# Optimization experiments

Measured on AMD Instinct MI355X. Metric: run time of the kernel, lower is better.

## Reference

```python
import jax, jax.numpy as jnp
import numpy as np

B, S, D, H = 2, 4096, 512, 4  # batch, seq, hidden, broadcast heads (mask shape)
SCALE = np.float32(np.sqrt(D))  # original divides by np.sqrt(self.d)


def setup_inputs() -> dict:
    key = jax.random.key(0)
    ks = jax.random.split(key, 7)
    lim = np.float32(1.0 / np.sqrt(D))  # torch Linear default init range
    return {
        "q": jax.random.normal(ks[0], (B, S, D), dtype=jnp.float32),
        "k": jax.random.normal(ks[1], (B, S, D), dtype=jnp.float32),
        "v": jax.random.normal(ks[2], (B, S, D), dtype=jnp.float32),
        "Wq": jax.random.uniform(ks[3], (D, D), jnp.float32, -lim, lim),
        "bq": jax.random.uniform(ks[4], (D,), jnp.float32, -lim, lim),
        "Wv": jax.random.uniform(ks[5], (D, D), jnp.float32, -lim, lim),
        "bv": jax.random.uniform(ks[6], (D,), jnp.float32, -lim, lim),
    }


def reference(q, k, v, Wq, bq, Wv, bv):
    # Q projection (original only projects q; key/value raw k is used for scores)
    Q = q @ Wq.T + bq                                   # [B,S,D]
    scores = jnp.einsum("bsd,btd->bst", Q, k) / SCALE   # [B,S,S]
    # zero attn_mask of shape [B,H,S,S] broadcasts scores to [B,H,S,S]
    scores = jnp.broadcast_to(scores[:, None, :, :], (B, H, S, S))
    attn = jax.nn.softmax(scores, axis=-1)              # [B,H,S,S]
    V = v @ Wv.T + bv                                   # [B,S,D]
    out = jnp.einsum("bhst,btd->bhsd", attn, V)         # [B,H,S,D]
    return out
```

## Files before the change

### kernel.cpp

```cpp
#include <hip/hip_runtime.h>
#include <math.h>

#define SEQ 4096
#define DIM 512
#define NBATCH 2

typedef __bf16 bf16;
typedef __bf16 bf16x8 __attribute__((ext_vector_type(8)));
typedef __bf16 bf16x4 __attribute__((ext_vector_type(4)));
typedef float  f32x4  __attribute__((ext_vector_type(4)));

#define GLOAD_LDS16(g, l)                                                              \
  __builtin_amdgcn_global_load_lds((__attribute__((address_space(1))) void*)(g),       \
                                   (__attribute__((address_space(3))) void*)(l), 16, 0, 0)

static const long NQ_ = (long)NBATCH * SEQ * DIM;
static const long NW_ = (long)DIM * DIM;
#define QSCALE 0.04419417382415922f

__device__ __forceinline__ void cvt4(const float* __restrict__ s, bf16* __restrict__ d) {
  f32x4 x = *(const f32x4*)s;
  bf16x4 y;
  y[0] = (bf16)x[0]; y[1] = (bf16)x[1]; y[2] = (bf16)x[2]; y[3] = (bf16)x[3];
  *(bf16x4*)d = y;
}

__global__ __launch_bounds__(256)
void cast5(const float* __restrict__ q, const float* __restrict__ k,
           const float* __restrict__ v, const float* __restrict__ Wq,
           const float* __restrict__ Wv,
           bf16* __restrict__ qb, bf16* __restrict__ kb, bf16* __restrict__ vb,
           bf16* __restrict__ wqb, bf16* __restrict__ wvb) {
  long tid = blockIdx.x * 256L + threadIdx.x;
  long nth = gridDim.x * 256L;
  for (long i = tid * 4; i < NQ_; i += nth * 4) {
    cvt4(q + i, qb + i);
    cvt4(k + i, kb + i);
    cvt4(v + i, vb + i);
  }
  for (long i = tid * 4; i < NW_; i += nth * 4) {
    cvt4(Wq + i, wqb + i);
    cvt4(Wv + i, wvb + i);
  }
}

__global__ __launch_bounds__(256)
void zero_f32(float* __restrict__ p, int n) {
  int i = blockIdx.x * 256 + threadIdx.x;
  if (i < n) p[i] = 0.0f;
}

template <int OUT>
__global__ __launch_bounds__(512, 2)
void gemm8(const bf16* __restrict__ A, const bf16* __restrict__ Bt,
           void* __restrict__ Cv, const float* __restrict__ bias0,
           const float* __restrict__ bias1, float* __restrict__ rowsum,
           int N, int K, long sB) {
  __shared__ __align__(16) bf16 lA[2][256 * 64];
  __shared__ __align__(16) bf16 lB[2][128 * 64];
  const int t = threadIdx.x;
  const int l = t & 63, w = t >> 6;

  const unsigned bid = blockIdx.y * gridDim.x + blockIdx.x;
  const unsigned nwg = gridDim.x * gridDim.y;
  const unsigned q8 = nwg >> 3;
  const unsigned swz = (bid & 7) * q8 + (bid >> 3);
  const long m0 = (long)(swz % gridDim.x) * 256;
  const long n0 = (long)(swz / gridDim.x) * 128;

  const int z = blockIdx.z;
  if constexpr (OUT == 0) {
    A += (long)z * NQ_;
    Bt += (long)z * NW_;
  } else {
    Bt += (m0 >> 12) * sB;
  }

  const int wr = (w >> 1) * 64;
  const int wc = (w & 1) * 64;
  const int lr = l & 15, lg = l >> 4;

  const bf16* gA[4];
  const bf16* gB[2];
#pragma unroll
  for (int i = 0; i < 4; ++i) {
    int s = i * 512 + t, row = s >> 3, kc = (s & 7) ^ (row & 7);
    gA[i] = A + (m0 + row) * (long)K + kc * 8;
  }
#pragma unroll
  for (int i = 0; i < 2; ++i) {
    int s = i * 512 + t, row = s >> 3, kc = (s & 7) ^ (row & 7);
    gB[i] = Bt + (n0 + row) * (long)K + kc * 8;
  }

  int offA[4][2], offB[4][2];
#pragma unroll
  for (int m = 0; m < 4; ++m)
#pragma unroll
    for (int ks = 0; ks < 2; ++ks)
      offA[m][ks] = (wr + m * 16 + lr) * 64 + (((ks * 4 + lg) ^ (lr & 7)) * 8);
#pragma unroll
  for (int n = 0; n < 4; ++n)
#pragma unroll
    for (int ks = 0; ks < 2; ++ks)
      offB[n][ks] = (wc + n * 16 + lr) * 64 + (((ks * 4 + lg) ^ (lr & 7)) * 8);

  auto stage6 = [&](long koff, bf16* dA, bf16* dB) {
#pragma unroll
    for (int i = 0; i < 4; ++i) GLOAD_LDS16(gA[i] + koff, dA + (i * 512 + w * 64) * 8);
#pragma unroll
    for (int i = 0; i < 2; ++i) GLOAD_LDS16(gB[i] + koff, dB + (i * 512 + w * 64) * 8);
  };

  f32x4 acc[4][4] = {};
  const int NT = K >> 6;

  stage6(0, lA[0], lB[0]);
  stage6(64, lA[1], lB[1]);
  asm volatile("s_waitcnt vmcnt(6)" ::: "memory");
  __builtin_amdgcn_sched_barrier(0);
  __builtin_amdgcn_s_barrier();
  __builtin_amdgcn_sched_barrier(0);

  for (int tt = 0; tt < NT; ++tt) {
    const int cur = tt & 1;
    const bf16* bufA = lA[cur];
    const bf16* bufB = lB[cur];
    bf16x8 a0[4], b0[4];
#pragma unroll
    for (int m = 0; m < 4; ++m) a0[m] = *(const bf16x8*)(bufA + offA[m][0]);
#pragma unroll
    for (int n = 0; n < 4; ++n) b0[n] = *(const bf16x8*)(bufB + offB[n][0]);
    asm volatile("s_waitcnt lgkmcnt(0)" ::: "memory");
    __builtin_amdgcn_sched_barrier(0);
    __builtin_amdgcn_s_setprio(1);
#pragma unroll
    for (int m = 0; m < 4; ++m)
#pragma unroll
      for (int n = 0; n < 4; ++n)
        acc[m][n] = __builtin_amdgcn_mfma_f32_16x16x32_bf16(a0[m], b0[n], acc[m][n], 0, 0, 0);
    __builtin_amdgcn_s_setprio(0);
    bf16x8 a1[4], b1[4];
#pragma unroll
    for (int m = 0; m < 4; ++m) a1[m] = *(const bf16x8*)(bufA + offA[m][1]);
#pragma unroll
    for (int n = 0; n < 4; ++n) b1[n] = *(const bf16x8*)(bufB + offB[n][1]);
    asm volatile("s_waitcnt lgkmcnt(0)" ::: "memory");
    __builtin_amdgcn_sched_barrier(0);
    __builtin_amdgcn_s_barrier();
    __builtin_amdgcn_sched_barrier(0);
    if (tt + 2 < NT) stage6((long)(tt + 2) * 64, lA[cur], lB[cur]);
    __builtin_amdgcn_s_setprio(1);
#pragma unroll
    for (int m = 0; m < 4; ++m)
#pragma unroll
      for (int n = 0; n < 4; ++n)
        acc[m][n] = __builtin_amdgcn_mfma_f32_16x16x32_bf16(a1[m], b1[n], acc[m][n], 0, 0, 0);
    __builtin_amdgcn_s_setprio(0);
    if (tt + 2 < NT) {
      asm volatile("s_waitcnt vmcnt(6)" ::: "memory");
    } else if (tt + 1 < NT) {
      asm volatile("s_waitcnt vmcnt(0)" ::: "memory");
    }
    if (tt + 1 < NT) {
      __builtin_amdgcn_sched_barrier(0);
      __builtin_amdgcn_s_barrier();
      __builtin_amdgcn_sched_barrier(0);
    }
  }

  if constexpr (OUT == 0) {
    if (z == 0) {
      bf16* C = (bf16*)Cv;
#pragma unroll
      for (int n = 0; n < 4; ++n) {
        const long col = n0 + wc + n * 16 + lr;
        const float bcol = bias0[col];
#pragma unroll
        for (int m = 0; m < 4; ++m) {
          const long rowb = m0 + wr + m * 16 + lg * 4;
#pragma unroll
          for (int r = 0; r < 4; ++r)
            C[(rowb + r) * (long)DIM + col] = (bf16)((acc[m][n][r] + bcol) * QSCALE);
        }
      }
    } else {
      bf16* Vt = (bf16*)Cv + NQ_;
#pragma unroll
      for (int n = 0; n < 4; ++n) {
        const long col = n0 + wc + n * 16 + lr;
        const float bcol = bias1[col];
#pragma unroll
        for (int m = 0; m < 4; ++m) {
          const long rowb = m0 + wr + m * 16 + lg * 4;
#pragma unroll
          for (int r = 0; r < 4; ++r) {
            long gr = rowb + r, bb = gr >> 12, ss = gr & 4095;
            Vt[bb * (long)(DIM * SEQ) + col * (long)SEQ + ss] = (bf16)(acc[m][n][r] + bcol);
          }
        }
      }
    }
  } else if constexpr (OUT == 1) {
    bf16* C = (bf16*)Cv;
#pragma unroll
    for (int m = 0; m < 4; ++m) {
      const long rowb = m0 + wr + m * 16 + lg * 4;
#pragma unroll
      for (int r = 0; r < 4; ++r) {
        float rsum = 0.0f;
#pragma unroll
        for (int n = 0; n < 4; ++n) {
          const long col = n0 + wc + n * 16 + lr;
          float e = __expf(acc[m][n][r]);
          bf16 eb = (bf16)e;
          C[(rowb + r) * (long)N + col] = eb;
          rsum += (float)eb;
        }
        rsum += __shfl_xor(rsum, 1);
        rsum += __shfl_xor(rsum, 2);
        rsum += __shfl_xor(rsum, 4);
        rsum += __shfl_xor(rsum, 8);
        if (lr == 0) atomicAdd(rowsum + rowb + r, rsum);
      }
    }
  } else {
    float* o = (float*)Cv;
#pragma unroll
    for (int m = 0; m < 4; ++m) {
      const long rowb = m0 + wr + m * 16 + lg * 4;
#pragma unroll
      for (int r = 0; r < 4; ++r) {
        const long gr = rowb + r, bb = gr >> 12, ss = gr & 4095;
        const float inv = 1.0f / rowsum[gr];
        float* p0 = o + bb * (4L * SEQ * DIM) + ss * (long)DIM;
#pragma unroll
        for (int n = 0; n < 4; ++n) {
          const long col = n0 + wc + n * 16 + lr;
          float vv = acc[m][n][r] * inv;
          p0[col] = vv;
          p0[col + 1L * SEQ * DIM] = vv;
          p0[col + 2L * SEQ * DIM] = vv;
          p0[col + 3L * SEQ * DIM] = vv;
        }
      }
    }
  }
}

extern "C" void kernel_launch(void* const* d_in, const int* in_sizes, int n_in,
                              void* d_out, int out_size, void* d_ws, size_t ws_size,
                              hipStream_t stream) {
  const float* q  = (const float*)d_in[0];
  const float* k  = (const float*)d_in[1];
  const float* v  = (const float*)d_in[2];
  const float* Wq = (const float*)d_in[3];
  const float* bq = (const float*)d_in[4];
  const float* Wv = (const float*)d_in[5];
  const float* bv = (const float*)d_in[6];
  float* outp = (float*)d_out;

  bf16* Qbf = (bf16*)d_ws;
  bf16* Vt  = Qbf + NQ_;
  bf16* Kbf = Vt + NQ_;
  bf16* Wqb = Kbf + NQ_;
  bf16* Wvb = Wqb + NW_;
  bf16* Sbuf = Wvb + NW_;
  const size_t baseBytes = (size_t)((char*)Sbuf - (char*)d_ws);
  const bool batched = ws_size >= baseBytes + 2ULL * SEQ * SEQ * 2;
  bf16* qb = Sbuf;
  bf16* vb = Sbuf + NQ_;
  float* rowsum = (float*)Wqb;

  const long sQK = (long)SEQ * DIM;
  const long sO  = 4L * SEQ * DIM;

  cast5<<<dim3(2048), dim3(256), 0, stream>>>(q, k, v, Wq, Wv, qb, Kbf, vb, Wqb, Wvb);
  gemm8<0><<<dim3(32, 4, 2), dim3(512), 0, stream>>>(
      qb, Wqb, Qbf, bq, bv, nullptr, 512, 512, 0);
  if (batched) {
    zero_f32<<<dim3(32), dim3(256), 0, stream>>>(rowsum, NBATCH * SEQ);
    gemm8<1><<<dim3(32, 32, 1), dim3(512), 0, stream>>>(
        Qbf, Kbf, Sbuf, nullptr, nullptr, rowsum, 4096, 512, sQK);
    gemm8<2><<<dim3(32, 4, 1), dim3(512), 0, stream>>>(
        Sbuf, Vt, outp, nullptr, nullptr, rowsum, 512, 4096, sQK);
  } else {
    for (int b = 0; b < 2; ++b) {
      zero_f32<<<dim3(16), dim3(256), 0, stream>>>(rowsum, SEQ);
      gemm8<1><<<dim3(16, 32, 1), dim3(512), 0, stream>>>(
          Qbf + b * sQK, Kbf + b * sQK, Sbuf, nullptr, nullptr, rowsum, 4096, 512, sQK);
      gemm8<2><<<dim3(16, 4, 1), dim3(512), 0, stream>>>(
          Sbuf, Vt + b * sQK, outp + b * sO, nullptr, nullptr, rowsum, 512, 4096, sQK);
    }
  }
}
```

Before: 278.1 us.

## Template GEMM on tile shape with triple-buffered BK=32 LDS pipeline

Replaces the fixed 256x128 double-buffered BK=64 GEMM with a templated BMxBN kernel that uses a three-stage LDS ring of BK=32 tiles. Each iteration issues the next global-to-LDS load before the MFMAs and needs only one barrier per step. Tile shapes are chosen per stage: 128x128 for the projections and the PV product, which doubles the grid, and 256x256 for the score GEMM. The catch is more loop iterations with smaller K slices, and the bigger score tiles hold more accumulators, which may limit occupancy.

```diff
diff --git a/kernel.cpp b/kernel.cpp
--- a/kernel.cpp
+++ b/kernel.cpp
@@ -13,6 +13,8 @@
 #define GLOAD_LDS16(g, l)                                                              \
   __builtin_amdgcn_global_load_lds((__attribute__((address_space(1))) void*)(g),       \
                                    (__attribute__((address_space(3))) void*)(l), 16, 0, 0)
+
+#define VMCNT(n) asm volatile("s_waitcnt vmcnt(" #n ")" ::: "memory")
 
 static const long NQ_ = (long)NBATCH * SEQ * DIM;
 static const long NW_ = (long)DIM * DIM;
@@ -50,23 +52,31 @@
   if (i < n) p[i] = 0.0f;
 }
 
-template <int OUT>
-__global__ __launch_bounds__(512, 2)
-void gemm8(const bf16* __restrict__ A, const bf16* __restrict__ Bt,
+template <int BM, int BN, int OUT>
+__global__ __launch_bounds__(512, (BM == 256 ? 2 : 4))
+void gemm3(const bf16* __restrict__ A, const bf16* __restrict__ Bt,
            void* __restrict__ Cv, const float* __restrict__ bias0,
            const float* __restrict__ bias1, float* __restrict__ rowsum,
            int N, int K, long sB) {
-  __shared__ __align__(16) bf16 lA[2][256 * 64];
-  __shared__ __align__(16) bf16 lB[2][128 * 64];
+  constexpr int MF = BM / 32;
+  constexpr int NF = BN / 64;
+  constexpr int LA = BM / 128;
+  constexpr int LB = BN / 128;
+  constexpr int NLD = LA + LB;
+  constexpr int ASZ = BM * 32;
+  constexpr int BSZ = BN * 32;
+  __shared__ __align__(16) bf16 lds[3][ASZ + BSZ];
+
   const int t = threadIdx.x;
   const int l = t & 63, w = t >> 6;
+  const int lr = l & 15, lg = l >> 4;
 
   const unsigned bid = blockIdx.y * gridDim.x + blockIdx.x;
   const unsigned nwg = gridDim.x * gridDim.y;
   const unsigned q8 = nwg >> 3;
   const unsigned swz = (bid & 7) * q8 + (bid >> 3);
-  const long m0 = (long)(swz % gridDim.x) * 256;
-  const long n0 = (long)(swz / gridDim.x) * 128;
+  const long m0 = (long)(swz % gridDim.x) * BM;
+  const long n0 = (long)(swz / gridDim.x) * BN;
 
   const int z = blockIdx.z;
   if constexpr (OUT == 0) {
@@ -76,127 +86,132 @@
     Bt += (m0 >> 12) * sB;
   }
 
-  const int wr = (w >> 1) * 64;
-  const int wc = (w & 1) * 64;
-  const int lr = l & 15, lg = l >> 4;
-
-  const bf16* gA[4];
-  const bf16* gB[2];
-#pragma unroll
-  for (int i = 0; i < 4; ++i) {
-    int s = i * 512 + t, row = s >> 3, kc = (s & 7) ^ (row & 7);
-    gA[i] = A + (m0 + row) * (long)K + kc * 8;
-  }
-#pragma unroll
-  for (int i = 0; i < 2; ++i) {
-    int s = i * 512 + t, row = s >> 3, kc = (s & 7) ^ (row & 7);
-    gB[i] = Bt + (n0 + row) * (long)K + kc * 8;
-  }
-
-  int offA[4][2], offB[4][2];
-#pragma unroll
-  for (int m = 0; m < 4; ++m)
-#pragma unroll
-    for (int ks = 0; ks < 2; ++ks)
-      offA[m][ks] = (wr + m * 16 + lr) * 64 + (((ks * 4 + lg) ^ (lr & 7)) * 8);
-#pragma unroll
-  for (int n = 0; n < 4; ++n)
-#pragma unroll
-    for (int ks = 0; ks < 2; ++ks)
-      offB[n][ks] = (wc + n * 16 + lr) * 64 + (((ks * 4 + lg) ^ (lr & 7)) * 8);
-
-  auto stage6 = [&](long koff, bf16* dA, bf16* dB) {
-#pragma unroll
-    for (int i = 0; i < 4; ++i) GLOAD_LDS16(gA[i] + koff, dA + (i * 512 + w * 64) * 8);
-#pragma unroll
-    for (int i = 0; i < 2; ++i) GLOAD_LDS16(gB[i] + koff, dB + (i * 512 + w * 64) * 8);
+  const int wr = (w >> 2) * (BM / 2);
+  const int wc = (w & 3) * (BN / 4);
+
+  const bf16* gA[LA];
+  const bf16* gB[LB];
+#pragma unroll
+  for (int i = 0; i < LA; ++i) {
+    int s = i * 512 + t, row = s >> 2, c = (s & 3) ^ ((row >> 1) & 3);
+    gA[i] = A + (m0 + row) * (long)K + c * 8;
+  }
+#pragma unroll
+  for (int i = 0; i < LB; ++i) {
+    int s = i * 512 + t, row = s >> 2, c = (s & 3) ^ ((row >> 1) & 3);
+    gB[i] = Bt + (n0 + row) * (long)K + c * 8;
+  }
+
+  int offA[MF], offB[NF];
+#pragma unroll
+  for (int mf = 0; mf < MF; ++mf)
+    offA[mf] = (wr + mf * 16 + lr) * 32 + ((lg ^ ((lr >> 1) & 3)) * 8);
+#pragma unroll
+  for (int nf = 0; nf < NF; ++nf)
+    offB[nf] = ASZ + (wc + nf * 16 + lr) * 32 + ((lg ^ ((lr >> 1) & 3)) * 8);
+
+  auto stage = [&](int tt, int bidx) {
+    const long ko = (long)tt * 32;
+#pragma unroll
+    for (int i = 0; i < LA; ++i)
+      GLOAD_LDS16(gA[i] + ko, &lds[bidx][(i * 512 + w * 64) * 8]);
+#pragma unroll
+    for (int i = 0; i < LB; ++i)
+      GLOAD_LDS16(gB[i] + ko, &lds[bidx][ASZ + (i * 512 + w * 64) * 8]);
   };
 
-  f32x4 acc[4][4] = {};
-  const int NT = K >> 6;
-
-  stage6(0, lA[0], lB[0]);
-  stage6(64, lA[1], lB[1]);
-  asm volatile("s_waitcnt vmcnt(6)" ::: "memory");
+  f32x4 acc[MF][NF] = {};
+  const int NT = K >> 5;
+
+  stage(0, 0);
+  stage(1, 1);
+  if constexpr (NLD == 4) VMCNT(4); else VMCNT(2);
   __builtin_amdgcn_sched_barrier(0);
   __builtin_amdgcn_s_barrier();
   __builtin_amdgcn_sched_barrier(0);
 
-  for (int tt = 0; tt < NT; ++tt) {
-    const int cur = tt & 1;
-    const bf16* bufA = lA[cur];
-    const bf16* bufB = lB[cur];
-    bf16x8 a0[4], b0[4];
-#pragma unroll
-    for (int m = 0; m < 4; ++m) a0[m] = *(const bf16x8*)(bufA + offA[m][0]);
-#pragma unroll
-    for (int n = 0; n < 4; ++n) b0[n] = *(const bf16x8*)(bufB + offB[n][0]);
-    asm volatile("s_waitcnt lgkmcnt(0)" ::: "memory");
-    __builtin_amdgcn_sched_barrier(0);
+  int cur = 0, stg = 2;
+  for (int tt = 0; tt < NT - 2; ++tt) {
+    bf16x8 af[MF], bfn[NF];
+#pragma unroll
+    for (int mf = 0; mf < MF; ++mf) af[mf] = *(const bf16x8*)(&lds[cur][offA[mf]]);
+#pragma unroll
+    for (int nf = 0; nf < NF; ++nf) bfn[nf] = *(const bf16x8*)(&lds[cur][offB[nf]]);
+    stage(tt + 2, stg);
     __builtin_amdgcn_s_setprio(1);
 #pragma unroll
-    for (int m = 0; m < 4; ++m)
-#pragma unroll
-      for (int n = 0; n < 4; ++n)
-        acc[m][n] = __builtin_amdgcn_mfma_f32_16x16x32_bf16(a0[m], b0[n], acc[m][n], 0, 0, 0);
+    for (int mf = 0; mf < MF; ++mf)
+#pragma unroll
+      for (int nf = 0; nf < NF; ++nf)
+        acc[mf][nf] = __builtin_amdgcn_mfma_f32_16x16x32_bf16(af[mf], bfn[nf], acc[mf][nf], 0, 0, 0);
     __builtin_amdgcn_s_setprio(0);
-    bf16x8 a1[4], b1[4];
-#pragma unroll
-    for (int m = 0; m < 4; ++m) a1[m] = *(const bf16x8*)(bufA + offA[m][1]);
-#pragma unroll
-    for (int n = 0; n < 4; ++n) b1[n] = *(const bf16x8*)(bufB + offB[n][1]);
-    asm volatile("s_waitcnt lgkmcnt(0)" ::: "memory");
+    if constexpr (NLD == 4) VMCNT(4); else VMCNT(2);
     __builtin_amdgcn_sched_barrier(0);
     __builtin_amdgcn_s_barrier();
     __builtin_amdgcn_sched_barrier(0);
-    if (tt + 2 < NT) stage6((long)(tt + 2) * 64, lA[cur], lB[cur]);
+    cur = (cur == 2) ? 0 : cur + 1;
+    stg = (stg == 2) ? 0 : stg + 1;
+  }
+  {
+    bf16x8 af[MF], bfn[NF];
+#pragma unroll
+    for (int mf = 0; mf < MF; ++mf) af[mf] = *(const bf16x8*)(&lds[cur][offA[mf]]);
+#pragma unroll
+    for (int nf = 0; nf < NF; ++nf) bfn[nf] = *(const bf16x8*)(&lds[cur][offB[nf]]);
     __builtin_amdgcn_s_setprio(1);
 #pragma unroll
-    for (int m = 0; m < 4; ++m)
-#pragma unroll
-      for (int n = 0; n < 4; ++n)
-        acc[m][n] = __builtin_amdgcn_mfma_f32_16x16x32_bf16(a1[m], b1[n], acc[m][n], 0, 0, 0);
+    for (int mf = 0; mf < MF; ++mf)
+#pragma unroll
+      for (int nf = 0; nf < NF; ++nf)
+        acc[mf][nf] = __builtin_amdgcn_mfma_f32_16x16x32_bf16(af[mf], bfn[nf], acc[mf][nf], 0, 0, 0);
     __builtin_amdgcn_s_setprio(0);
-    if (tt + 2 < NT) {
-      asm volatile("s_waitcnt vmcnt(6)" ::: "memory");
-    } else if (tt + 1 < NT) {
-      asm volatile("s_waitcnt vmcnt(0)" ::: "memory");
-    }
-    if (tt + 1 < NT) {
-      __builtin_amdgcn_sched_barrier(0);
-      __builtin_amdgcn_s_barrier();
-      __builtin_amdgcn_sched_barrier(0);
-    }
+    VMCNT(0);
+    __builtin_amdgcn_sched_barrier(0);
+    __builtin_amdgcn_s_barrier();
+    __builtin_amdgcn_sched_barrier(0);
+    cur = (cur == 2) ? 0 : cur + 1;
+  }
+  {
+    bf16x8 af[MF], bfn[NF];
+#pragma unroll
+    for (int mf = 0; mf < MF; ++mf) af[mf] = *(const bf16x8*)(&lds[cur][offA[mf]]);
+#pragma unroll
+    for (int nf = 0; nf < NF; ++nf) bfn[nf] = *(const bf16x8*)(&lds[cur][offB[nf]]);
+#pragma unroll
+    for (int mf = 0; mf < MF; ++mf)
+#pragma unroll
+      for (int nf = 0; nf < NF; ++nf)
+        acc[mf][nf] = __builtin_amdgcn_mfma_f32_16x16x32_bf16(af[mf], bfn[nf], acc[mf][nf], 0, 0, 0);
   }
 
   if constexpr (OUT == 0) {
     if (z == 0) {
       bf16* C = (bf16*)Cv;
 #pragma unroll
-      for (int n = 0; n < 4; ++n) {
-        const long col = n0 + wc + n * 16 + lr;
+      for (int nf = 0; nf < NF; ++nf) {
+        const long col = n0 + wc + nf * 16 + lr;
         const float bcol = bias0[col];
 #pragma unroll
-        for (int m = 0; m < 4; ++m) {
-          const long rowb = m0 + wr + m * 16 + lg * 4;
+        for (int mf = 0; mf < MF; ++mf) {
+          const long rowb = m0 + wr + mf * 16 + lg * 4;
 #pragma unroll
           for (int r = 0; r < 4; ++r)
-            C[(rowb + r) * (long)DIM + col] = (bf16)((acc[m][n][r] + bcol) * QSCALE);
+            C[(rowb + r) * (long)DIM + col] = (bf16)((acc[mf][nf][r] + bcol) * QSCALE);
         }
       }
     } else {
       bf16* Vt = (bf16*)Cv + NQ_;
 #pragma unroll
-      for (int n = 0; n < 4; ++n) {
-        const long col = n0 + wc + n * 16 + lr;
+      for (int nf = 0; nf < NF; ++nf) {
+        const long col = n0 + wc + nf * 16 + lr;
         const float bcol = bias1[col];
 #pragma unroll
-        for (int m = 0; m < 4; ++m) {
-          const long rowb = m0 + wr + m * 16 + lg * 4;
+        for (int mf = 0; mf < MF; ++mf) {
+          const long rowb = m0 + wr + mf * 16 + lg * 4;
 #pragma unroll
           for (int r = 0; r < 4; ++r) {
             long gr = rowb + r, bb = gr >> 12, ss = gr & 4095;
-            Vt[bb * (long)(DIM * SEQ) + col * (long)SEQ + ss] = (bf16)(acc[m][n][r] + bcol);
+            Vt[bb * (long)(DIM * SEQ) + col * (long)SEQ + ss] = (bf16)(acc[mf][nf][r] + bcol);
           }
         }
       }
@@ -204,15 +219,15 @@
   } else if constexpr (OUT == 1) {
     bf16* C = (bf16*)Cv;
 #pragma unroll
-    for (int m = 0; m < 4; ++m) {
-      const long rowb = m0 + wr + m * 16 + lg * 4;
+    for (int mf = 0; mf < MF; ++mf) {
+      const long rowb = m0 + wr + mf * 16 + lg * 4;
 #pragma unroll
       for (int r = 0; r < 4; ++r) {
         float rsum = 0.0f;
 #pragma unroll
-        for (int n = 0; n < 4; ++n) {
-          const long col = n0 + wc + n * 16 + lr;
-          float e = __expf(acc[m][n][r]);
+        for (int nf = 0; nf < NF; ++nf) {
+          const long col = n0 + wc + nf * 16 + lr;
+          float e = __expf(acc[mf][nf][r]);
           bf16 eb = (bf16)e;
           C[(rowb + r) * (long)N + col] = eb;
           rsum += (float)eb;
@@ -227,17 +242,17 @@
   } else {
     float* o = (float*)Cv;
 #pragma unroll
-    for (int m = 0; m < 4; ++m) {
-      const long rowb = m0 + wr + m * 16 + lg * 4;
+    for (int mf = 0; mf < MF; ++mf) {
+      const long rowb = m0 + wr + mf * 16 + lg * 4;
 #pragma unroll
       for (int r = 0; r < 4; ++r) {
         const long gr = rowb + r, bb = gr >> 12, ss = gr & 4095;
         const float inv = 1.0f / rowsum[gr];
         float* p0 = o + bb * (4L * SEQ * DIM) + ss * (long)DIM;
 #pragma unroll
-        for (int n = 0; n < 4; ++n) {
-          const long col = n0 + wc + n * 16 + lr;
-          float vv = acc[m][n][r] * inv;
+        for (int nf = 0; nf < NF; ++nf) {
+          const long col = n0 + wc + nf * 16 + lr;
+          float vv = acc[mf][nf][r] * inv;
           p0[col] = vv;
           p0[col + 1L * SEQ * DIM] = vv;
           p0[col + 2L * SEQ * DIM] = vv;
@@ -276,20 +291,20 @@
   const long sO  = 4L * SEQ * DIM;
 
   cast5<<<dim3(2048), dim3(256), 0, stream>>>(q, k, v, Wq, Wv, qb, Kbf, vb, Wqb, Wvb);
-  gemm8<0><<<dim3(32, 4, 2), dim3(512), 0, stream>>>(
+  gemm3<128, 128, 0><<<dim3(64, 4, 2), dim3(512), 0, stream>>>(
       qb, Wqb, Qbf, bq, bv, nullptr, 512, 512, 0);
   if (batched) {
     zero_f32<<<dim3(32), dim3(256), 0, stream>>>(rowsum, NBATCH * SEQ);
-    gemm8<1><<<dim3(32, 32, 1), dim3(512), 0, stream>>>(
+    gemm3<256, 256, 1><<<dim3(32, 16, 1), dim3(512), 0, stream>>>(
         Qbf, Kbf, Sbuf, nullptr, nullptr, rowsum, 4096, 512, sQK);
-    gemm8<2><<<dim3(32, 4, 1), dim3(512), 0, stream>>>(
+    gemm3<128, 128, 2><<<dim3(64, 4, 1), dim3(512), 0, stream>>>(
         Sbuf, Vt, outp, nullptr, nullptr, rowsum, 512, 4096, sQK);
   } else {
     for (int b = 0; b < 2; ++b) {
       zero_f32<<<dim3(16), dim3(256), 0, stream>>>(rowsum, SEQ);
-      gemm8<1><<<dim3(16, 32, 1), dim3(512), 0, stream>>>(
+      gemm3<256, 256, 1><<<dim3(16, 16, 1), dim3(512), 0, stream>>>(
           Qbf + b * sQK, Kbf + b * sQK, Sbuf, nullptr, nullptr, rowsum, 4096, 512, sQK);
-      gemm8<2><<<dim3(16, 4, 1), dim3(512), 0, stream>>>(
+      gemm3<128, 128, 2><<<dim3(32, 4, 1), dim3(512), 0, stream>>>(
           Sbuf, Vt + b * sQK, outp + b * sO, nullptr, nullptr, rowsum, 512, 4096, sQK);
     }
   }
```

Result: faster. 231.1 us (-16.9%).
